# Kernel optimization log

Hardware: AMD Instinct MI355X
Metric: run time of the kernel (lower is better)

Reference implementation:

```python
import jax, jax.numpy as jnp
import numpy as np

B, T, C, H = 2, 2048, 1024, 16
HS = C // H  # 64
EPS = 1e-5


def layer_norm(x, w, b):
    mu = jnp.mean(x, axis=-1, keepdims=True)
    var = jnp.var(x, axis=-1, keepdims=True)
    return (x - mu) * jax.lax.rsqrt(var + EPS) * w + b


def setup_inputs() -> dict:
    key = jax.random.key(0)
    ks = jax.random.split(key, 16)
    s_c = 1.0 / np.sqrt(C)
    s_f = 1.0 / np.sqrt(4 * C)
    u = lambda k, shape, s: jax.random.uniform(k, shape, jnp.float32, -s, s)
    return {
        "x": jax.random.normal(ks[0], (B, T, C), jnp.float32),
        # per-head Q/K/V Linears stacked over heads: [H, C, HS], bias [H, HS]
        "Wq": u(ks[1], (H, C, HS), s_c), "bq": u(ks[2], (H, HS), s_c),
        "Wk": u(ks[3], (H, C, HS), s_c), "bk": u(ks[4], (H, HS), s_c),
        "Wv": u(ks[5], (H, C, HS), s_c), "bv": u(ks[6], (H, HS), s_c),
        "Wp": u(ks[7], (C, C), s_c), "bp": u(ks[8], (C,), s_c),
        "W1": u(ks[9], (C, 4 * C), s_c), "b1": u(ks[10], (4 * C,), s_c),
        "W2": u(ks[11], (4 * C, C), s_f), "b2": u(ks[12], (C,), s_f),
        "ln1_w": jnp.ones((C,), jnp.float32), "ln1_b": jnp.zeros((C,), jnp.float32),
        "ln2_w": jnp.ones((C,), jnp.float32), "ln2_b": jnp.zeros((C,), jnp.float32),
    }


def reference(x, Wq, bq, Wk, bk, Wv, bv, Wp, bp, W1, b1, W2, b2,
              ln1_w, ln1_b, ln2_w, ln2_b):
    # --- pre-norm self-attention ---
    xn = layer_norm(x, ln1_w, ln1_b)
    q = jnp.einsum('btc,hcd->bhtd', xn, Wq) + bq[None, :, None, :]
    k = jnp.einsum('btc,hcd->bhtd', xn, Wk) + bk[None, :, None, :]
    v = jnp.einsum('btc,hcd->bhtd', xn, Wv) + bv[None, :, None, :]
    # NOTE: original scales by C**-0.5 (full embedding dim), not head_size**-0.5
    att = jnp.einsum('bhtd,bhsd->bhts', q, k) * (C ** -0.5)
    att = jax.nn.softmax(att, axis=-1)
    o = jnp.einsum('bhts,bhsd->bhtd', att, v)  # [B,H,T,HS]
    o = jnp.transpose(o, (0, 2, 1, 3)).reshape(B, T, C)  # concat heads
    sa = o @ Wp + bp
    out = x + sa
    # --- pre-norm FFN (exact erf GELU, matching nn.GELU default) ---
    on = layer_norm(out, ln2_w, ln2_b)
    h = jax.nn.gelu(on @ W1 + b1, approximate=False)
    return out + (h @ W2 + b2)
```

## Files before the change

kernel.cpp:

```cpp
#include <hip/hip_runtime.h>
#include <math.h>

#define BB 2
#define TT 2048
#define CC 1024
#define HH 16
#define HS 64
#define MT 4096
#define FF 4096

typedef unsigned short u16;
typedef __bf16 bfrag __attribute__((ext_vector_type(8)));
typedef float f4 __attribute__((ext_vector_type(4)));
typedef float f16v __attribute__((ext_vector_type(16)));

#define AS1(p) ((const __attribute__((address_space(1))) void*)(p))
#define AS3(p) ((__attribute__((address_space(3))) void*)(p))

__device__ __forceinline__ u16 f2bf(float f) {
  union { float f; unsigned u; } a; a.f = f;
  return (u16)((a.u + 0x7fffu + ((a.u >> 16) & 1u)) >> 16);
}
__device__ __forceinline__ float bf2f(u16 u) {
  union { unsigned u; float f; } a; a.u = ((unsigned)u) << 16; return a.f;
}

__device__ __forceinline__ int swz128(int byteoff) {
  return byteoff ^ (((byteoff >> 7) & 7) << 4);
}
__device__ __forceinline__ int swzAB(int byteoff) {
  return byteoff ^ (((byteoff >> 7) & 3) << 4);
}

#define XCD_SWZ_2D(BX, BY)                                                     \
  int _fl = (int)blockIdx.y * gridDim.x + blockIdx.x;                          \
  const int _nw = gridDim.x * gridDim.y;                                       \
  _fl = (_fl & 7) * (_nw >> 3) + (_fl >> 3);                                   \
  const int BX = _fl % gridDim.x;                                              \
  const int BY = _fl / gridDim.x;

__global__ void tr_f32_bf16(const float* __restrict__ src, u16* __restrict__ dst,
                            int R, int Cc, long long sb, long long db, int dld) {
  __shared__ float t[32][33];
  const int bz = blockIdx.z;
  const int r0 = blockIdx.y * 32, c0 = blockIdx.x * 32;
  const int tx = threadIdx.x, ty = threadIdx.y;
  const float* s = src + bz * sb;
  u16* d = dst + bz * db;
#pragma unroll
  for (int i = 0; i < 4; i++)
    t[ty + i * 8][tx] = s[(size_t)(r0 + ty + i * 8) * Cc + c0 + tx];
  __syncthreads();
#pragma unroll
  for (int i = 0; i < 4; i++)
    d[(size_t)(c0 + ty + i * 8) * dld + r0 + tx] = f2bf(t[tx][ty + i * 8]);
}

__global__ void tr_bf16(const u16* __restrict__ src, u16* __restrict__ dst,
                        int R, int Cc, long long sb, long long db, int dld) {
  __shared__ u16 t[32][33];
  const int bz = blockIdx.z;
  const int r0 = blockIdx.y * 32, c0 = blockIdx.x * 32;
  const int tx = threadIdx.x, ty = threadIdx.y;
  const u16* s = src + bz * sb;
  u16* d = dst + bz * db;
#pragma unroll
  for (int i = 0; i < 4; i++)
    t[ty + i * 8][tx] = s[(size_t)(r0 + ty + i * 8) * Cc + c0 + tx];
  __syncthreads();
#pragma unroll
  for (int i = 0; i < 4; i++)
    d[(size_t)(c0 + ty + i * 8) * dld + r0 + tx] = t[tx][ty + i * 8];
}

__global__ __launch_bounds__(256) void ln_kernel(
    const float* __restrict__ x, const float* __restrict__ w,
    const float* __restrict__ b, u16* __restrict__ y) {
  const int row = blockIdx.x, tid = threadIdx.x;
  const float4 v = reinterpret_cast<const float4*>(x + (size_t)row * CC)[tid];
  float s = v.x + v.y + v.z + v.w;
  float s2 = v.x * v.x + v.y * v.y + v.z * v.z + v.w * v.w;
#pragma unroll
  for (int off = 32; off >= 1; off >>= 1) {
    s += __shfl_xor(s, off);
    s2 += __shfl_xor(s2, off);
  }
  __shared__ float ps[4], ps2[4];
  const int wave = tid >> 6, lane = tid & 63;
  if (lane == 0) { ps[wave] = s; ps2[wave] = s2; }
  __syncthreads();
  s = ps[0] + ps[1] + ps[2] + ps[3];
  s2 = ps2[0] + ps2[1] + ps2[2] + ps2[3];
  const float mu = s * (1.f / CC);
  const float rstd = rsqrtf(s2 * (1.f / CC) - mu * mu + 1e-5f);
  const float4 wv = reinterpret_cast<const float4*>(w)[tid];
  const float4 bv = reinterpret_cast<const float4*>(b)[tid];
  ushort4 o;
  o.x = f2bf((v.x - mu) * rstd * wv.x + bv.x);
  o.y = f2bf((v.y - mu) * rstd * wv.y + bv.y);
  o.z = f2bf((v.z - mu) * rstd * wv.z + bv.z);
  o.w = f2bf((v.w - mu) * rstd * wv.w + bv.w);
  reinterpret_cast<ushort4*>(y + (size_t)row * CC)[tid] = o;
}

template<int NJ>
__device__ __forceinline__ void gemm_core(
    u16* smem, const u16* __restrict__ A, const u16* __restrict__ Bt,
    int K, int lda, int ldb, int bmi, int bni, f4 (&acc)[4][NJ]) {
  constexpr int BN = NJ * 32;
  constexpr int BBUF = BN * 32;
  u16* As = smem;
  u16* Bs = smem + 3 * 4096;
  const int tid = threadIdx.x;
  const int wave = tid >> 6, lane = tid & 63;
  const int wm = wave >> 1, wn = wave & 1;
  const int lg = lane >> 4, ll = lane & 15;

  const int trow = tid >> 2;
  const int tch  = (tid & 3) ^ ((trow >> 1) & 3);
  const u16* ga = A + (size_t)(bmi * 128 + trow) * lda + tch * 8;
  const u16* gb = Bt + (size_t)(bni * BN + trow) * ldb + tch * 8;
  const size_t g64a = (size_t)64 * lda;
  const size_t g64b = (size_t)64 * ldb;
  const int nt = K >> 5;

  auto GSTAGE = [&](int bi, int kt) {
    u16* la = &As[bi * 4096 + tid * 8];
    u16* lb = &Bs[bi * BBUF + tid * 8];
    const u16* gA = ga + kt * 32;
    const u16* gB = gb + kt * 32;
    __builtin_amdgcn_global_load_lds(AS1(gA), AS3(la), 16, 0, 0);
    __builtin_amdgcn_global_load_lds(AS1(gA + g64a), AS3(la + 2048), 16, 0, 0);
    __builtin_amdgcn_global_load_lds(AS1(gB), AS3(lb), 16, 0, 0);
    if constexpr (NJ == 4)
      __builtin_amdgcn_global_load_lds(AS1(gB + g64b), AS3(lb + 2048), 16, 0, 0);
  };

  GSTAGE(0, 0);
  GSTAGE(1, 1);
  GSTAGE(2, 2);
  int bi = 0;
  for (int t = 0; t < nt; t++) {
    const int ahead = nt - 1 - t;
    if constexpr (NJ == 4) {
      if (ahead >= 2)      asm volatile("s_waitcnt vmcnt(8)" ::: "memory");
      else if (ahead == 1) asm volatile("s_waitcnt vmcnt(4)" ::: "memory");
      else                 asm volatile("s_waitcnt vmcnt(0)" ::: "memory");
    } else {
      if (ahead >= 2)      asm volatile("s_waitcnt vmcnt(6)" ::: "memory");
      else if (ahead == 1) asm volatile("s_waitcnt vmcnt(3)" ::: "memory");
      else                 asm volatile("s_waitcnt vmcnt(0)" ::: "memory");
    }
    __builtin_amdgcn_s_barrier();
    __builtin_amdgcn_sched_barrier(0);

    const char* as_ = (const char*)(As + bi * 4096);
    const char* bs_ = (const char*)(Bs + bi * BBUF);
    bfrag af[4], bf[NJ];
#pragma unroll
    for (int i = 0; i < 4; i++)
      af[i] = *(const bfrag*)(as_ + swzAB((wm * 64 + i * 16 + ll) * 64 + lg * 16));
#pragma unroll
    for (int j = 0; j < NJ; j++)
      bf[j] = *(const bfrag*)(bs_ + swzAB((wn * (BN / 2) + j * 16 + ll) * 64 + lg * 16));

    __builtin_amdgcn_s_setprio(1);
#pragma unroll
    for (int i = 0; i < 4; i++)
#pragma unroll
      for (int j = 0; j < NJ; j++)
        acc[i][j] = __builtin_amdgcn_mfma_f32_16x16x32_bf16(af[i], bf[j], acc[i][j], 0, 0, 0);
    __builtin_amdgcn_s_setprio(0);

    __builtin_amdgcn_sched_barrier(0);
    __builtin_amdgcn_s_barrier();
    if (t + 3 < nt) GSTAGE(bi, t + 3);
    bi = (bi == 2) ? 0 : bi + 1;
  }
}

#define EPI_COORDS                                              \
  const int tid = threadIdx.x;                                  \
  const int wave = tid >> 6, lane = tid & 63;                   \
  const int wm = wave >> 1, wn = wave & 1;                      \
  const int lg = lane >> 4, ll = lane & 15;

__global__ __launch_bounds__(256, 3) void gemm_qkv(
    const u16* __restrict__ A, const u16* __restrict__ Bt,
    const float* __restrict__ bq, const float* __restrict__ bk,
    const float* __restrict__ bv,
    u16* __restrict__ q, u16* __restrict__ k, u16* __restrict__ v) {
  __shared__ u16 smem[24576];
  XCD_SWZ_2D(bx, by)
  f4 acc[4][4] = {};
  gemm_core<4>(smem, A, Bt, CC, CC, CC, by, bx, acc);
  EPI_COORDS
  __syncthreads();
#pragma unroll
  for (int j = 0; j < 4; j++) {
    const int n = bx * 128 + wn * 64 + j * 16 + ll;
    const int sec = n >> 10, nn = n & 1023;
    const float bias = (sec == 0 ? bq : (sec == 1 ? bk : bv))[nn];
    const float scale = (sec == 0) ? 0.045084220027780106f : 1.0f;
#pragma unroll
    for (int i = 0; i < 4; i++)
#pragma unroll
      for (int r = 0; r < 4; r++)
        smem[(wm * 64 + i * 16 + lg * 4 + r) * 136 + wn * 64 + j * 16 + ll] =
            f2bf((acc[i][j][r] + bias) * scale);
  }
  __syncthreads();
  const int rr = tid >> 4, cb = (tid & 15) * 8;
#pragma unroll
  for (int R = 0; R < 8; R++) {
    const int row = R * 16 + rr;
    const int m = by * 128 + row, b = m >> 11, t = m & 2047;
    const int n = bx * 128 + cb;
    const int sec = n >> 10, nn = n & 1023, h = nn >> 6, d = nn & 63;
    u16* dst = sec == 0 ? q : (sec == 1 ? k : v);
    *(uint4*)&dst[(((size_t)b * HH + h) * TT + t) * HS + d] =
        *(const uint4*)&smem[row * 136 + cb];
  }
}

__global__ __launch_bounds__(256, 3) void gemm_ffn1(
    const u16* __restrict__ A, const u16* __restrict__ Bt,
    const float* __restrict__ b1, u16* __restrict__ hb) {
  __shared__ u16 smem[24576];
  XCD_SWZ_2D(bx, by)
  f4 acc[4][4] = {};
  gemm_core<4>(smem, A, Bt, CC, CC, CC, by, bx, acc);
  EPI_COORDS
  __syncthreads();
#pragma unroll
  for (int j = 0; j < 4; j++) {
    const int n = bx * 128 + wn * 64 + j * 16 + ll;
    const float bias = b1[n];
#pragma unroll
    for (int i = 0; i < 4; i++)
#pragma unroll
      for (int r = 0; r < 4; r++) {
        const float t = acc[i][j][r] + bias;
        const float g = 0.5f * t * (1.0f + erff(t * 0.70710678118654752f));
        smem[(wm * 64 + i * 16 + lg * 4 + r) * 136 + wn * 64 + j * 16 + ll] = f2bf(g);
      }
  }
  __syncthreads();
  const int rr = tid >> 4, cb = (tid & 15) * 8;
#pragma unroll
  for (int R = 0; R < 8; R++) {
    const int row = R * 16 + rr;
    *(uint4*)&hb[(size_t)(by * 128 + row) * FF + bx * 128 + cb] =
        *(const uint4*)&smem[row * 136 + cb];
  }
}

__global__ __launch_bounds__(256, 3) void gemm_ffn2sk(
    const u16* __restrict__ A, const u16* __restrict__ Bt,
    u16* __restrict__ p0, u16* __restrict__ p1) {
  __shared__ u16 smem[24576];
  int _fl = ((int)blockIdx.z * gridDim.y + blockIdx.y) * gridDim.x + blockIdx.x;
  const int _nw = gridDim.x * gridDim.y * gridDim.z;
  _fl = (_fl & 7) * (_nw >> 3) + (_fl >> 3);
  const int bx = _fl % gridDim.x;
  const int by = (_fl / gridDim.x) % gridDim.y;
  const int bz = _fl / (gridDim.x * gridDim.y);

  f4 acc[4][4] = {};
  gemm_core<4>(smem, A + bz * 2048, Bt + bz * 2048, 2048, FF, FF, by, bx, acc);
  EPI_COORDS
  __syncthreads();
#pragma unroll
  for (int j = 0; j < 4; j++)
#pragma unroll
    for (int i = 0; i < 4; i++)
#pragma unroll
      for (int r = 0; r < 4; r++)
        smem[(wm * 64 + i * 16 + lg * 4 + r) * 136 + wn * 64 + j * 16 + ll] =
            f2bf(acc[i][j][r]);
  __syncthreads();
  u16* pp = bz ? p1 : p0;
  const int rr = tid >> 4, cb = (tid & 15) * 8;
#pragma unroll
  for (int R = 0; R < 8; R++) {
    const int row = R * 16 + rr;
    *(uint4*)&pp[(size_t)(by * 128 + row) * CC + bx * 128 + cb] =
        *(const uint4*)&smem[row * 136 + cb];
  }
}

__global__ __launch_bounds__(256) void ffn2_reduce(
    const u16* __restrict__ p0, const u16* __restrict__ p1,
    const float* __restrict__ b2, float* __restrict__ dout) {
  const int gid = blockIdx.x * 256 + threadIdx.x;
  const int n0 = (gid * 8) & (CC - 1);
  const uint4 a = ((const uint4*)p0)[gid];
  const uint4 c = ((const uint4*)p1)[gid];
  const u16* au = (const u16*)&a;
  const u16* cu = (const u16*)&c;
  float4 d0 = ((const float4*)dout)[gid * 2];
  float4 d1 = ((const float4*)dout)[gid * 2 + 1];
  const float4 w0 = *(const float4*)&b2[n0];
  const float4 w1 = *(const float4*)&b2[n0 + 4];
  d0.x += w0.x + bf2f(au[0]) + bf2f(cu[0]);
  d0.y += w0.y + bf2f(au[1]) + bf2f(cu[1]);
  d0.z += w0.z + bf2f(au[2]) + bf2f(cu[2]);
  d0.w += w0.w + bf2f(au[3]) + bf2f(cu[3]);
  d1.x += w1.x + bf2f(au[4]) + bf2f(cu[4]);
  d1.y += w1.y + bf2f(au[5]) + bf2f(cu[5]);
  d1.z += w1.z + bf2f(au[6]) + bf2f(cu[6]);
  d1.w += w1.w + bf2f(au[7]) + bf2f(cu[7]);
  ((float4*)dout)[gid * 2] = d0;
  ((float4*)dout)[gid * 2 + 1] = d1;
}

__global__ __launch_bounds__(256, 3) void gemm_proj(
    const u16* __restrict__ A, const u16* __restrict__ Bt,
    const float* __restrict__ bp, const float* __restrict__ x,
    float* __restrict__ outw) {
  __shared__ u16 smem[18432];
  XCD_SWZ_2D(bx, by)
  f4 acc[4][2] = {};
  gemm_core<2>(smem, A, Bt, CC, CC, CC, by, bx, acc);
  EPI_COORDS
#pragma unroll
  for (int i = 0; i < 4; i++)
#pragma unroll
    for (int j = 0; j < 2; j++) {
      const int n = bx * 64 + wn * 32 + j * 16 + ll;
      const float bias = bp[n];
#pragma unroll
      for (int r = 0; r < 4; r++) {
        const int m = by * 128 + wm * 64 + i * 16 + lg * 4 + r;
        const size_t idx = (size_t)m * CC + n;
        outw[idx] = acc[i][j][r] + bias + x[idx];
      }
    }
}

__global__ __launch_bounds__(256, 2) void attn_kernel(
    const u16* __restrict__ Q, const u16* __restrict__ Kb,
    const u16* __restrict__ Vt, u16* __restrict__ Ao) {
  __shared__ __align__(1024) u16 Ks[2][128 * 64];
  __shared__ __align__(1024) u16 Vs[2][2][64 * 64];

  const int fl = (int)blockIdx.y * gridDim.x + blockIdx.x;
  const int idx = fl >> 3;
  const int bh = (idx >> 4) * 8 + (fl & 7);
  const int qt = idx & 15;

  const int tid = threadIdx.x, wave = tid >> 6, lane = tid & 63;
  const int l31 = lane & 31, hi = lane >> 5;

  bfrag qf[4];
  const u16* Qb = Q + ((size_t)bh * TT + qt * 128 + wave * 32) * HS;
#pragma unroll
  for (int t = 0; t < 4; t++)
    qf[t] = *(const bfrag*)&Qb[l31 * HS + t * 16 + hi * 8];

  f16v o0 = {}, o1 = {};
  float lrun = 0.f;

  const int trow = tid >> 3;
  const int tch  = (tid & 7) ^ (trow & 7);
  const u16* gk = Kb + ((size_t)bh * TT + trow) * HS + tch * 8;
  const u16* gv = Vt + ((size_t)bh * HS + trow) * TT + tch * 8;

  int koff[4][4], voff[2][2][2];
#pragma unroll
  for (int sub = 0; sub < 4; sub++)
#pragma unroll
    for (int t = 0; t < 4; t++)
      koff[sub][t] = swz128((sub * 32 + l31) * 128 + t * 32 + hi * 16);
#pragma unroll
  for (int sh = 0; sh < 2; sh++)
#pragma unroll
    for (int dh = 0; dh < 2; dh++)
#pragma unroll
      for (int ks = 0; ks < 2; ks++)
        voff[dh][sh][ks] = swz128((dh * 32 + l31) * 128 + sh * 64 + ks * 32 + hi * 16);

  const f16v zseed = {};

#define STAGE(bufi, stt)                                                          \
  do {                                                                            \
    u16* lk = &Ks[bufi][tid * 8];                                                 \
    __builtin_amdgcn_global_load_lds(AS1(gk + (size_t)(stt) * HS), AS3(lk), 16, 0, 0); \
    __builtin_amdgcn_global_load_lds(AS1(gk + (size_t)((stt) + 32) * HS), AS3(lk + 2048), 16, 0, 0); \
    __builtin_amdgcn_global_load_lds(AS1(gk + (size_t)((stt) + 64) * HS), AS3(lk + 4096), 16, 0, 0); \
    __builtin_amdgcn_global_load_lds(AS1(gk + (size_t)((stt) + 96) * HS), AS3(lk + 6144), 16, 0, 0); \
    u16* lv0 = &Vs[bufi][0][tid * 8];                                             \
    u16* lv1 = &Vs[bufi][1][tid * 8];                                             \
    __builtin_amdgcn_global_load_lds(AS1(gv + (stt)), AS3(lv0), 16, 0, 0);        \
    __builtin_amdgcn_global_load_lds(AS1(gv + (stt) + (size_t)32 * TT), AS3(lv0 + 2048), 16, 0, 0); \
    __builtin_amdgcn_global_load_lds(AS1(gv + (stt) + 64), AS3(lv1), 16, 0, 0);   \
    __builtin_amdgcn_global_load_lds(AS1(gv + (stt) + 64 + (size_t)32 * TT), AS3(lv1 + 2048), 16, 0, 0); \
  } while (0)

  STAGE(0, 0);
  int cur = 0;

  for (int st = 0; st < TT; st += 128) {
    if (st + 128 < TT) {
      STAGE(cur ^ 1, st + 128);
      asm volatile("s_waitcnt vmcnt(8)" ::: "memory");
    } else {
      asm volatile("s_waitcnt vmcnt(0)" ::: "memory");
    }
    __builtin_amdgcn_s_barrier();
    __builtin_amdgcn_sched_barrier(0);

    const char* kbuf = (const char*)Ks[cur];

    f16v s[4];
#pragma unroll
    for (int sub = 0; sub < 4; sub++) {
      s[sub] = __builtin_amdgcn_mfma_f32_32x32x16_bf16(
          *(const bfrag*)(kbuf + koff[sub][0]), qf[0], zseed, 0, 0, 0);
#pragma unroll
      for (int t = 1; t < 4; t++) {
        const bfrag kf = *(const bfrag*)(kbuf + koff[sub][t]);
        s[sub] = __builtin_amdgcn_mfma_f32_32x32x16_bf16(kf, qf[t], s[sub], 0, 0, 0);
      }
    }

    float rs = 0.f;
#pragma unroll
    for (int sub = 0; sub < 4; sub++) {
#pragma unroll
      for (int j = 0; j < 16; j++) s[sub][j] = exp2f(s[sub][j]);
      float p8[8];
#pragma unroll
      for (int j = 0; j < 8; j++) p8[j] = s[sub][j] + s[sub][j + 8];
#pragma unroll
      for (int j = 0; j < 4; j++) p8[j] += p8[j + 4];
      rs += (p8[0] + p8[1]) + (p8[2] + p8[3]);

      unsigned a0, a1, a2, a3, a4, a5, a6, a7;
      asm("v_cvt_pk_bf16_f32 %0, %1, %2" : "=v"(a0) : "v"(s[sub][0]),  "v"(s[sub][1]));
      asm("v_cvt_pk_bf16_f32 %0, %1, %2" : "=v"(a1) : "v"(s[sub][2]),  "v"(s[sub][3]));
      asm("v_cvt_pk_bf16_f32 %0, %1, %2" : "=v"(a2) : "v"(s[sub][4]),  "v"(s[sub][5]));
      asm("v_cvt_pk_bf16_f32 %0, %1, %2" : "=v"(a3) : "v"(s[sub][6]),  "v"(s[sub][7]));
      asm("v_cvt_pk_bf16_f32 %0, %1, %2" : "=v"(a4) : "v"(s[sub][8]),  "v"(s[sub][9]));
      asm("v_cvt_pk_bf16_f32 %0, %1, %2" : "=v"(a5) : "v"(s[sub][10]), "v"(s[sub][11]));
      asm("v_cvt_pk_bf16_f32 %0, %1, %2" : "=v"(a6) : "v"(s[sub][12]), "v"(s[sub][13]));
      asm("v_cvt_pk_bf16_f32 %0, %1, %2" : "=v"(a7) : "v"(s[sub][14]), "v"(s[sub][15]));
      asm("v_permlane32_swap_b32 %0, %1" : "+v"(a2), "+v"(a0));
      asm("v_permlane32_swap_b32 %0, %1" : "+v"(a3), "+v"(a1));
      asm("v_permlane32_swap_b32 %0, %1" : "+v"(a6), "+v"(a4));
      asm("v_permlane32_swap_b32 %0, %1" : "+v"(a7), "+v"(a5));

      const char* vb_ = (const char*)Vs[cur][sub >> 1];
      {
        union { unsigned u[4]; bfrag b; } pb;
        pb.u[0] = a0; pb.u[1] = a1; pb.u[2] = a2; pb.u[3] = a3;
        const bfrag vf0 = *(const bfrag*)(vb_ + voff[0][sub & 1][0]);
        o0 = __builtin_amdgcn_mfma_f32_32x32x16_bf16(vf0, pb.b, o0, 0, 0, 0);
        const bfrag vf1 = *(const bfrag*)(vb_ + voff[1][sub & 1][0]);
        o1 = __builtin_amdgcn_mfma_f32_32x32x16_bf16(vf1, pb.b, o1, 0, 0, 0);
      }
      {
        union { unsigned u[4]; bfrag b; } pb;
        pb.u[0] = a4; pb.u[1] = a5; pb.u[2] = a6; pb.u[3] = a7;
        const bfrag vf0 = *(const bfrag*)(vb_ + voff[0][sub & 1][1]);
        o0 = __builtin_amdgcn_mfma_f32_32x32x16_bf16(vf0, pb.b, o0, 0, 0, 0);
        const bfrag vf1 = *(const bfrag*)(vb_ + voff[1][sub & 1][1]);
        o1 = __builtin_amdgcn_mfma_f32_32x32x16_bf16(vf1, pb.b, o1, 0, 0, 0);
      }
    }
    rs += __shfl_xor(rs, 32);
    lrun += rs;

    __builtin_amdgcn_sched_barrier(0);
    __builtin_amdgcn_s_barrier();
    cur ^= 1;
  }
#undef STAGE

  const int b = bh >> 4, h = bh & 15;
  const float inv = 1.0f / lrun;
  const int t = qt * 128 + wave * 32 + l31;
  u16* aorow = Ao + ((size_t)b * TT + t) * CC + h * HS;
#pragma unroll
  for (int dh = 0; dh < 2; dh++) {
    const f16v& ov = dh ? o1 : o0;
#pragma unroll
    for (int rq = 0; rq < 4; rq++) {
      union { uint2 v; __bf16 hh[4]; } w;
      w.hh[0] = (__bf16)(ov[rq * 4 + 0] * inv);
      w.hh[1] = (__bf16)(ov[rq * 4 + 1] * inv);
      w.hh[2] = (__bf16)(ov[rq * 4 + 2] * inv);
      w.hh[3] = (__bf16)(ov[rq * 4 + 3] * inv);
      *(uint2*)&aorow[dh * 32 + rq * 8 + hi * 4] = w.v;
    }
  }
}

extern "C" void kernel_launch(void* const* d_in, const int* in_sizes, int n_in,
                              void* d_out, int out_size, void* d_ws, size_t ws_size,
                              hipStream_t stream) {
  const float* x    = (const float*)d_in[0];
  const float* Wq   = (const float*)d_in[1];
  const float* bq   = (const float*)d_in[2];
  const float* Wk   = (const float*)d_in[3];
  const float* bk   = (const float*)d_in[4];
  const float* Wv   = (const float*)d_in[5];
  const float* bv   = (const float*)d_in[6];
  const float* Wp   = (const float*)d_in[7];
  const float* bp   = (const float*)d_in[8];
  const float* W1   = (const float*)d_in[9];
  const float* b1   = (const float*)d_in[10];
  const float* W2   = (const float*)d_in[11];
  const float* b2   = (const float*)d_in[12];
  const float* ln1w = (const float*)d_in[13];
  const float* ln1b = (const float*)d_in[14];
  const float* ln2w = (const float*)d_in[15];
  const float* ln2b = (const float*)d_in[16];
  float* dout = (float*)d_out;

  char* ws = (char*)d_ws;
  u16* wqkv = (u16*)(ws + 0);
  u16* wpt  = (u16*)(ws + 6291456);
  u16* w1t  = (u16*)(ws + 8388608);
  u16* w2t  = (u16*)(ws + 16777216);
  u16* xn   = (u16*)(ws + 25165824);
  u16* qb   = (u16*)(ws + 33554432);
  u16* kb   = (u16*)(ws + 41943040);
  u16* vb   = (u16*)(ws + 50331648);
  u16* vt   = (u16*)(ws + 58720256);
  u16* ao   = (u16*)(ws + 67108864);
  u16* hb   = qb;
  u16* pk0  = (u16*)(ws + 0);
  u16* pk1  = (u16*)(ws + 8388608);

  dim3 blk256(256);
  dim3 blkT(32, 8);

  tr_f32_bf16<<<dim3(2, 32, 16), blkT, 0, stream>>>(Wq, wqkv,               1024,   64, 65536LL, 65536LL, 1024);
  tr_f32_bf16<<<dim3(2, 32, 16), blkT, 0, stream>>>(Wk, wqkv + 1024 * 1024, 1024,   64, 65536LL, 65536LL, 1024);
  tr_f32_bf16<<<dim3(2, 32, 16), blkT, 0, stream>>>(Wv, wqkv + 2048 * 1024, 1024,   64, 65536LL, 65536LL, 1024);
  tr_f32_bf16<<<dim3(32, 32, 1),  blkT, 0, stream>>>(Wp, wpt, 1024, 1024, 0LL, 0LL, 1024);
  tr_f32_bf16<<<dim3(128, 32, 1), blkT, 0, stream>>>(W1, w1t, 1024, 4096, 0LL, 0LL, 1024);
  tr_f32_bf16<<<dim3(32, 128, 1), blkT, 0, stream>>>(W2, w2t, 4096, 1024, 0LL, 0LL, 4096);

  ln_kernel<<<dim3(MT), blk256, 0, stream>>>(x, ln1w, ln1b, xn);

  gemm_qkv<<<dim3(24, 32), blk256, 0, stream>>>(xn, wqkv, bq, bk, bv, qb, kb, vb);

  tr_bf16<<<dim3(2, 64, 32), blkT, 0, stream>>>(vb, vt, 2048, 64, 131072LL, 131072LL, 2048);

  attn_kernel<<<dim3(16, 32), blk256, 0, stream>>>(qb, kb, vt, ao);

  gemm_proj<<<dim3(16, 32), blk256, 0, stream>>>(ao, wpt, bp, x, dout);

  ln_kernel<<<dim3(MT), blk256, 0, stream>>>(dout, ln2w, ln2b, xn);

  gemm_ffn1<<<dim3(32, 32), blk256, 0, stream>>>(xn, w1t, b1, hb);
  gemm_ffn2sk<<<dim3(8, 32, 2), blk256, 0, stream>>>(hb, w2t, pk0, pk1);
  ffn2_reduce<<<dim3(MT * CC / 8 / 256), blk256, 0, stream>>>(pk0, pk1, b2, dout);
}
```

Before: 257.5 us.

## Write V transposed directly from QKV GEMM epilogue, drop separate transpose kernel

The QKV GEMM epilogue for V column blocks now writes bias-added V straight into the transposed [B,H,HS,T] layout, so the separate tr_bf16 transpose kernel and its launch are removed. This saves a full read and write of V plus one launch. The V stores are 8-byte scattered writes rather than staged 16-byte coalesced ones. Separately, the attention kernel moves the cross-half row-sum shuffle out of the inner loop into a single reduction after the loop.

```diff
diff --git a/kernel.cpp b/kernel.cpp
--- a/kernel.cpp
+++ b/kernel.cpp
@@ -54,23 +54,6 @@
 #pragma unroll
   for (int i = 0; i < 4; i++)
     d[(size_t)(c0 + ty + i * 8) * dld + r0 + tx] = f2bf(t[tx][ty + i * 8]);
-}
-
-__global__ void tr_bf16(const u16* __restrict__ src, u16* __restrict__ dst,
-                        int R, int Cc, long long sb, long long db, int dld) {
-  __shared__ u16 t[32][33];
-  const int bz = blockIdx.z;
-  const int r0 = blockIdx.y * 32, c0 = blockIdx.x * 32;
-  const int tx = threadIdx.x, ty = threadIdx.y;
-  const u16* s = src + bz * sb;
-  u16* d = dst + bz * db;
-#pragma unroll
-  for (int i = 0; i < 4; i++)
-    t[ty + i * 8][tx] = s[(size_t)(r0 + ty + i * 8) * Cc + c0 + tx];
-  __syncthreads();
-#pragma unroll
-  for (int i = 0; i < 4; i++)
-    d[(size_t)(c0 + ty + i * 8) * dld + r0 + tx] = t[tx][ty + i * 8];
 }
 
 __global__ __launch_bounds__(256) void ln_kernel(
@@ -189,18 +172,41 @@
     const u16* __restrict__ A, const u16* __restrict__ Bt,
     const float* __restrict__ bq, const float* __restrict__ bk,
     const float* __restrict__ bv,
-    u16* __restrict__ q, u16* __restrict__ k, u16* __restrict__ v) {
+    u16* __restrict__ q, u16* __restrict__ k, u16* __restrict__ vt) {
   __shared__ u16 smem[24576];
   XCD_SWZ_2D(bx, by)
   f4 acc[4][4] = {};
   gemm_core<4>(smem, A, Bt, CC, CC, CC, by, bx, acc);
   EPI_COORDS
+
+  if (bx >= 16) {
+    const int b = (by * 128) >> 11;
+    const int t0 = by * 128 + wm * 64;
+#pragma unroll
+    for (int j = 0; j < 4; j++) {
+      const int nn = (bx * 128 + wn * 64 + j * 16 + ll) & 1023;
+      const int h = nn >> 6, d = nn & 63;
+      const float bias = bv[nn];
+      u16* vrow = vt + ((size_t)(b * HH + h) * HS + d) * TT;
+#pragma unroll
+      for (int i = 0; i < 4; i++) {
+        union { uint2 v; __bf16 hh[4]; } w;
+        w.hh[0] = (__bf16)(acc[i][j][0] + bias);
+        w.hh[1] = (__bf16)(acc[i][j][1] + bias);
+        w.hh[2] = (__bf16)(acc[i][j][2] + bias);
+        w.hh[3] = (__bf16)(acc[i][j][3] + bias);
+        *(uint2*)&vrow[t0 + i * 16 + lg * 4] = w.v;
+      }
+    }
+    return;
+  }
+
   __syncthreads();
 #pragma unroll
   for (int j = 0; j < 4; j++) {
     const int n = bx * 128 + wn * 64 + j * 16 + ll;
     const int sec = n >> 10, nn = n & 1023;
-    const float bias = (sec == 0 ? bq : (sec == 1 ? bk : bv))[nn];
+    const float bias = (sec == 0 ? bq : bk)[nn];
     const float scale = (sec == 0) ? 0.045084220027780106f : 1.0f;
 #pragma unroll
     for (int i = 0; i < 4; i++)
@@ -217,7 +223,7 @@
     const int m = by * 128 + row, b = m >> 11, t = m & 2047;
     const int n = bx * 128 + cb;
     const int sec = n >> 10, nn = n & 1023, h = nn >> 6, d = nn & 63;
-    u16* dst = sec == 0 ? q : (sec == 1 ? k : v);
+    u16* dst = sec == 0 ? q : k;
     *(uint4*)&dst[(((size_t)b * HH + h) * TT + t) * HS + d] =
         *(const uint4*)&smem[row * 136 + cb];
   }
@@ -468,7 +474,6 @@
         o1 = __builtin_amdgcn_mfma_f32_32x32x16_bf16(vf1, pb.b, o1, 0, 0, 0);
       }
     }
-    rs += __shfl_xor(rs, 32);
     lrun += rs;
 
     __builtin_amdgcn_sched_barrier(0);
@@ -477,6 +482,7 @@
   }
 #undef STAGE
 
+  lrun += __shfl_xor(lrun, 32);
   const int b = bh >> 4, h = bh & 15;
   const float inv = 1.0f / lrun;
   const int t = qt * 128 + wave * 32 + l31;
@@ -526,7 +532,6 @@
   u16* xn   = (u16*)(ws + 25165824);
   u16* qb   = (u16*)(ws + 33554432);
   u16* kb   = (u16*)(ws + 41943040);
-  u16* vb   = (u16*)(ws + 50331648);
   u16* vt   = (u16*)(ws + 58720256);
   u16* ao   = (u16*)(ws + 67108864);
   u16* hb   = qb;
@@ -545,9 +550,7 @@
 
   ln_kernel<<<dim3(MT), blk256, 0, stream>>>(x, ln1w, ln1b, xn);
 
-  gemm_qkv<<<dim3(24, 32), blk256, 0, stream>>>(xn, wqkv, bq, bk, bv, qb, kb, vb);
-
-  tr_bf16<<<dim3(2, 64, 32), blkT, 0, stream>>>(vb, vt, 2048, 64, 131072LL, 131072LL, 2048);
+  gemm_qkv<<<dim3(24, 32), blk256, 0, stream>>>(xn, wqkv, bq, bk, bv, qb, kb, vt);
 
   attn_kernel<<<dim3(16, 32), blk256, 0, stream>>>(qb, kb, vt, ao);
 
```

Measured after the change: 252.9 us. Within noise of the previous version (-1.8%).
